# Kernel optimization log

Hardware: AMD Instinct MI355X
Metric: run time of the kernel (lower is better)

The kernel has to match this reference:

```python
import jax, jax.numpy as jnp
import numpy as np

B, T, C, H = 2, 2048, 1024, 16
D = C // H  # head dim 64

def setup_inputs() -> dict:
    key = jax.random.key(0)
    k1, k2, k3 = jax.random.split(key, 3)
    x = jax.random.normal(k1, (B, T, C), dtype=jnp.float32)
    W_attn = jax.random.normal(k2, (C, 3 * C), dtype=jnp.float32) * (1.0 / np.sqrt(C))
    b_attn = jnp.zeros((3 * C,), dtype=jnp.float32)
    W_proj = jax.random.normal(k3, (C, C), dtype=jnp.float32) * (1.0 / np.sqrt(C))
    b_proj = jnp.zeros((C,), dtype=jnp.float32)
    return {"x": x, "W_attn": W_attn, "b_attn": b_attn, "W_proj": W_proj, "b_proj": b_proj}

def reference(x, W_attn, b_attn, W_proj, b_proj):
    Bsz, Tlen, Cdim = x.shape
    qkv = x @ W_attn + b_attn  # [B,T,3C]
    q, k, v = jnp.split(qkv, 3, axis=2)
    # [B,T,C] -> [B,H,T,D]
    q = q.reshape(Bsz, Tlen, H, D).transpose(0, 2, 1, 3)
    k = k.reshape(Bsz, Tlen, H, D).transpose(0, 2, 1, 3)
    v = v.reshape(Bsz, Tlen, H, D).transpose(0, 2, 1, 3)
    att = jnp.einsum('bhqd,bhkd->bhqk', q, k) * (1.0 / np.sqrt(D))
    causal = jnp.tril(jnp.ones((Tlen, Tlen), dtype=bool))
    att = jnp.where(causal[None, None, :, :], att, jnp.float32(-jnp.inf))
    att = jax.nn.softmax(att, axis=-1)
    y = jnp.einsum('bhqk,bhkd->bhqd', att, v)  # [B,H,T,D]
    y = y.transpose(0, 2, 1, 3).reshape(Bsz, Tlen, Cdim)
    return y @ W_proj + b_proj
```

## Files before the change

kernel.cpp:

```cpp
#include <hip/hip_runtime.h>
#include <math.h>

#define BSZ 2
#define TSEQ 2048
#define CDIM 1024
#define HNUM 16

typedef __attribute__((ext_vector_type(8))) short bhalf8;
typedef __attribute__((ext_vector_type(4))) short bhalf4;
typedef __attribute__((ext_vector_type(4))) float floatx4;

__device__ __forceinline__ unsigned short f2bf(float f) {
    union { float f; unsigned u; } v;
    v.f = f;
    unsigned r = v.u + 0x7FFFu + ((v.u >> 16) & 1u);
    return (unsigned short)(r >> 16);
}

__device__ __forceinline__ floatx4 fx4_zero() { floatx4 z = {0.f,0.f,0.f,0.f}; return z; }

typedef __attribute__((address_space(3))) unsigned int lds_u32;
typedef const __attribute__((address_space(1))) unsigned int g_u32;
__device__ __forceinline__ void async_copy16(const void* g, void* l) {
    __builtin_amdgcn_global_load_lds((g_u32*)g, (lds_u32*)l, 16, 0, 0);
}

__device__ __forceinline__ void trans_tile(
    const float* __restrict__ W, unsigned short* __restrict__ Wt,
    int K, int N, int n0, int k0, int tid, float (*t)[33])
{
    const int tx = tid & 31, ty = tid >> 5;
#pragma unroll
    for (int i = 0; i < 4; ++i)
        t[ty + i * 8][tx] = W[(size_t)(k0 + ty + i * 8) * N + n0 + tx];
    __syncthreads();
#pragma unroll
    for (int i = 0; i < 4; ++i)
        Wt[(size_t)(n0 + ty + i * 8) * K + k0 + tx] = f2bf(t[tx][ty + i * 8]);
}

__global__ __launch_bounds__(256) void prepass(
    const float* __restrict__ x, unsigned short* __restrict__ xb,
    const float* __restrict__ Wa, unsigned short* __restrict__ WtA,
    const float* __restrict__ Wp, unsigned short* __restrict__ WtP)
{
    __shared__ float t[32][33];
    const int bid = blockIdx.x;
    const int tid = threadIdx.x;
    if (bid < 2048) {
        size_t i = ((size_t)bid * 256 + tid) * 8;
        float4 a = *(const float4*)(x + i);
        float4 b = *(const float4*)(x + i + 4);
        uint4 o;
        o.x = (unsigned)f2bf(a.x) | ((unsigned)f2bf(a.y) << 16);
        o.y = (unsigned)f2bf(a.z) | ((unsigned)f2bf(a.w) << 16);
        o.z = (unsigned)f2bf(b.x) | ((unsigned)f2bf(b.y) << 16);
        o.w = (unsigned)f2bf(b.z) | ((unsigned)f2bf(b.w) << 16);
        *(uint4*)(xb + i) = o;
    } else if (bid < 5120) {
        int tl = bid - 2048;
        trans_tile(Wa, WtA, 1024, 3072, (tl % 96) * 32, (tl / 96) * 32, tid, t);
    } else {
        int tl = bid - 5120;
        trans_tile(Wp, WtP, 1024, 1024, (tl % 32) * 32, (tl / 32) * 32, tid, t);
    }
}

template<int BM, int BN, int BK, bool OUT_BF16>
__global__ __launch_bounds__(256) void gemm_bt(
    const unsigned short* __restrict__ A, const unsigned short* __restrict__ Bt,
    const float* __restrict__ bias, void* __restrict__ Cp,
    int M, int N, int K, int v_start, unsigned short* __restrict__ vt, int q_end)
{
    constexpr int ALINES = (BM * BK) / 2048;
    constexpr int BLINES = (BN * BK) / 2048;
    constexpr int MT = BM / 32;
    constexpr int NT = BN / 32;
    constexpr int KK = BK / 32;
    constexpr int CPR = BK / 8;
    __shared__ unsigned short As[2][BM * BK];
    __shared__ unsigned short Bs[2][BN * BK];

    const int tid   = threadIdx.x;
    const int nx  = (int)gridDim.x;
    const int lin = (int)(blockIdx.y * gridDim.x + blockIdx.x);
    const int cpx = (int)(gridDim.x * gridDim.y) >> 3;
    const int swz = (lin & 7) * cpx + (lin >> 3);
    const int bn  = swz % nx;
    const int bm  = swz / nx;

    const int wave  = tid >> 6;
    const int col16 = tid & 15;
    const int quad  = (tid & 63) >> 4;
    const int wm    = (wave >> 1) * (BM / 2);
    const int wn    = (wave & 1) * (BN / 2);

    floatx4 acc[MT][NT];
#pragma unroll
    for (int i = 0; i < MT; ++i)
#pragma unroll
        for (int j = 0; j < NT; ++j) acc[i][j] = fx4_zero();

    const int gr = tid / CPR;
    const int cq = tid % CPR;
    const int gk = (BK == 32)
        ? (((cq + 4 - ((gr >> 1) & 3)) & 3) * 8)
        : ((cq ^ (gr & 7)) * 8);
    const unsigned short* Ab = A  + (size_t)(bm * BM + gr) * K + gk;
    const unsigned short* Bb = Bt + (size_t)(bn * BN + gr) * K + gk;
    constexpr int RPL = 2048 / BK;

#define STAGE(k0, bf) { \
    char* AsB = (char*)As[bf] + wave * 1024; \
    char* BsB = (char*)Bs[bf] + wave * 1024; \
    _Pragma("unroll") \
    for (int l = 0; l < ALINES; ++l) \
        async_copy16(Ab + (size_t)l * RPL * K + (k0), AsB + l * 4096); \
    _Pragma("unroll") \
    for (int l = 0; l < BLINES; ++l) \
        async_copy16(Bb + (size_t)l * RPL * K + (k0), BsB + l * 4096); }

#define COMPUTE(bf) { \
    _Pragma("unroll") \
    for (int kk = 0; kk < KK; ++kk) { \
        const int sw8 = (BK == 32) \
            ? (((quad + (col16 >> 1)) & 3) * 8) \
            : ((((kk << 2) + quad) ^ (col16 & 7)) * 8); \
        bhalf8 a[MT], b[NT]; \
        _Pragma("unroll") \
        for (int i = 0; i < MT; ++i) \
            a[i] = *(const bhalf8*)&As[bf][(wm + i * 16 + col16) * BK + sw8]; \
        _Pragma("unroll") \
        for (int j = 0; j < NT; ++j) \
            b[j] = *(const bhalf8*)&Bs[bf][(wn + j * 16 + col16) * BK + sw8]; \
        _Pragma("unroll") \
        for (int i = 0; i < MT; ++i) \
            _Pragma("unroll") \
            for (int j = 0; j < NT; ++j) \
                acc[i][j] = __builtin_amdgcn_mfma_f32_16x16x32_bf16(a[i], b[j], acc[i][j], 0, 0, 0); \
    } }

    STAGE(0, 0);
    __syncthreads();
    int buf = 0;
    for (int k0 = 0; k0 < K - BK; k0 += BK) {
        STAGE(k0 + BK, buf ^ 1);
        COMPUTE(buf);
        __syncthreads();
        buf ^= 1;
    }
    COMPUTE(buf);
#undef STAGE
#undef COMPUTE

    const int colbase = bn * BN + wn;
    const bool vpath = (v_start >= 0) && (colbase >= v_start);
    const float csc = (colbase < q_end) ? 0.18033688f : 1.0f;
#pragma unroll
    for (int j = 0; j < NT; ++j) {
        int col = colbase + j * 16 + col16;
        float bv = bias[col];
#pragma unroll
        for (int i = 0; i < MT; ++i) {
            if (vpath) {
                int row0 = bm * BM + wm + i * 16 + quad * 4;
                ushort4 o;
                o.x = f2bf((acc[i][j][0] + bv) * csc);
                o.y = f2bf((acc[i][j][1] + bv) * csc);
                o.z = f2bf((acc[i][j][2] + bv) * csc);
                o.w = f2bf((acc[i][j][3] + bv) * csc);
                size_t vrow = (size_t)((row0 >> 11) * 1024 + (col - v_start));
                *(ushort4*)(vt + vrow * 2048 + (row0 & 2047)) = o;
            } else {
#pragma unroll
                for (int r = 0; r < 4; ++r) {
                    int row = bm * BM + wm + i * 16 + quad * 4 + r;
                    float v = (acc[i][j][r] + bv) * csc;
                    if (OUT_BF16)
                        ((unsigned short*)Cp)[(size_t)row * N + col] = f2bf(v);
                    else
                        ((float*)Cp)[(size_t)row * N + col] = v;
                }
            }
        }
    }
}

template<bool DIAG>
__device__ __forceinline__ void attn_tile(
    const unsigned short* __restrict__ Ks, const unsigned short* __restrict__ Vt,
    const bhalf8* qf, floatx4* oT, floatx4& accl,
    int col16, int quad, int qloc)
{
    const int sx = col16 & 7;
    const floatx4 minusC = {-17.31234049f, -17.31234049f, -17.31234049f, -17.31234049f};
    const bhalf4 ones = {0x3F80, 0x3F80, 0x3F80, 0x3F80};

    floatx4 s[4];
#pragma unroll
    for (int n = 0; n < 4; ++n) {
        const int row = 16 * n + col16;
        bhalf8 k0 = *(const bhalf8*)&Ks[row * 64 + ((quad ^ sx) * 8)];
        bhalf8 k1 = *(const bhalf8*)&Ks[row * 64 + (((4 + quad) ^ sx) * 8)];
        floatx4 t = __builtin_amdgcn_mfma_f32_16x16x32_bf16(k0, qf[0], minusC, 0, 0, 0);
        s[n] = __builtin_amdgcn_mfma_f32_16x16x32_bf16(k1, qf[1], t, 0, 0, 0);
    }

    bhalf4 pb[4];
#pragma unroll
    for (int n = 0; n < 4; ++n) {
        unsigned a[4];
#pragma unroll
        for (int r = 0; r < 4; ++r) {
            float p = exp2f(s[n][r]);
            if (DIAG) {
                if (16 * n + quad * 4 + r > qloc) p = 0.f;
            }
            a[r] = __float_as_uint(p) + 0x8000u;
        }
        union { unsigned u[2]; bhalf4 b; } uu;
        uu.u[0] = (a[0] >> 16) | (a[1] & 0xffff0000u);
        uu.u[1] = (a[2] >> 16) | (a[3] & 0xffff0000u);
        pb[n] = uu.b;
        accl = __builtin_amdgcn_mfma_f32_16x16x16bf16_1k(ones, pb[n], accl, 0, 0, 0);
    }

#pragma unroll
    for (int n = 0; n < 4; ++n) {
#pragma unroll
        for (int dt = 0; dt < 4; ++dt) {
            const int d = 16 * dt + col16;
            const bhalf4 av = *(const bhalf4*)&Vt[d * 76 + 16 * n + quad * 4];
            oT[dt] = __builtin_amdgcn_mfma_f32_16x16x16bf16_1k(av, pb[n], oT[dt], 0, 0, 0);
        }
    }
}

__global__ __launch_bounds__(256) void attn_mfma(
    const unsigned short* __restrict__ qkv,
    const unsigned short* __restrict__ vT,
    unsigned short* __restrict__ yout)
{
    __shared__ unsigned short Kbuf[2][64 * 64];
    __shared__ unsigned short Vbuf[2][64 * 76];

    const int tid   = threadIdx.x;
    const int wave  = tid >> 6;
    const int col16 = tid & 15;
    const int quad  = (tid & 63) >> 4;

    const int y = (int)blockIdx.y;
    const int g = y >> 3, r = y & 7;
    const int qb = (g == 0) ? 31 - r : (g == 1) ? r : (g == 2) ? 23 - r : 8 + r;

    const int bh    = blockIdx.x;
    const int b     = bh >> 4;
    const int h     = bh & 15;

    const unsigned short* base  = qkv + (size_t)b * TSEQ * 3072 + h * 64;
    const unsigned short* kbase = base + CDIM;
    const unsigned short* vtb   = vT + (size_t)(b * 1024 + h * 64) * 2048;

    bhalf8 qf[2];
    {
        const unsigned short* qrow =
            base + (size_t)(qb * 64 + wave * 16 + col16) * 3072 + quad * 8;
        qf[0] = *(const bhalf8*)qrow;
        qf[1] = *(const bhalf8*)(qrow + 32);
    }

    const int krow = tid >> 3;
    const int kchk = (tid & 7) ^ (krow & 7);
    const unsigned short* ksrc0 = kbase + (size_t)krow * 3072 + kchk * 8;
    const unsigned short* ksrc1 = kbase + (size_t)(krow + 32) * 3072 + kchk * 8;

    const int vd  = tid >> 3;
    const int vt0 = (tid & 7) * 8;
    const unsigned short* vsrc0 = vtb + (size_t)vd * 2048 + vt0;
    const unsigned short* vsrc1 = vtb + (size_t)(vd + 32) * 2048 + vt0;

#define KSTAGE(kb, bf) { \
    char* Kd = (char*)Kbuf[bf] + wave * 1024; \
    async_copy16(ksrc0 + (size_t)(kb) * 64 * 3072, Kd); \
    async_copy16(ksrc1 + (size_t)(kb) * 64 * 3072, Kd + 4096); }

    floatx4 oT[4];
#pragma unroll
    for (int dt = 0; dt < 4; ++dt) oT[dt] = fx4_zero();
    floatx4 accl = fx4_zero();
    const int qloc = wave * 16 + col16;

    {
        uint4 nv0 = *(const uint4*)vsrc0;
        uint4 nv1 = *(const uint4*)vsrc1;
        KSTAGE(0, 0);
        *(uint4*)&Vbuf[0][vd * 76 + vt0]        = nv0;
        *(uint4*)&Vbuf[0][(vd + 32) * 76 + vt0] = nv1;
    }
    __syncthreads();
    int buf = 0;
    for (int kb = 0; kb < qb; ++kb) {
        uint4 nv0 = *(const uint4*)(vsrc0 + (size_t)(kb + 1) * 64);
        uint4 nv1 = *(const uint4*)(vsrc1 + (size_t)(kb + 1) * 64);
        KSTAGE(kb + 1, buf ^ 1);
        attn_tile<false>(Kbuf[buf], Vbuf[buf], qf, oT, accl, col16, quad, qloc);
        *(uint4*)&Vbuf[buf ^ 1][vd * 76 + vt0]        = nv0;
        *(uint4*)&Vbuf[buf ^ 1][(vd + 32) * 76 + vt0] = nv1;
        __syncthreads();
        buf ^= 1;
    }
    attn_tile<true>(Kbuf[buf], Vbuf[buf], qf, oT, accl, col16, quad, qloc);
#undef KSTAGE

    const float inv = 1.0f / accl[0];
    const size_t row = (size_t)b * TSEQ + (size_t)qb * 64 + wave * 16 + col16;
#pragma unroll
    for (int dt = 0; dt < 4; ++dt) {
        ushort4 o;
        o.x = f2bf(oT[dt][0] * inv);
        o.y = f2bf(oT[dt][1] * inv);
        o.z = f2bf(oT[dt][2] * inv);
        o.w = f2bf(oT[dt][3] * inv);
        *(ushort4*)(yout + row * CDIM + h * 64 + 16 * dt + quad * 4) = o;
    }
}

extern "C" void kernel_launch(void* const* d_in, const int* in_sizes, int n_in,
                              void* d_out, int out_size, void* d_ws, size_t ws_size,
                              hipStream_t stream)
{
    const float* x      = (const float*)d_in[0];
    const float* W_attn = (const float*)d_in[1];
    const float* b_attn = (const float*)d_in[2];
    const float* W_proj = (const float*)d_in[3];
    const float* b_proj = (const float*)d_in[4];
    float* out = (float*)d_out;

    unsigned short* qkv = (unsigned short*)d_ws;
    unsigned short* y   = qkv + (size_t)4096 * 3072;
    unsigned short* xb  = y   + (size_t)4096 * 1024;
    unsigned short* WtA = xb  + (size_t)4096 * 1024;
    unsigned short* WtP = WtA + (size_t)3072 * 1024;
    unsigned short* vT  = WtP + (size_t)1024 * 1024;

    prepass<<<dim3(6144), 256, 0, stream>>>(x, xb, W_attn, WtA, W_proj, WtP);

    gemm_bt<128, 128, 32, true><<<dim3(3072 / 128, 4096 / 128), 256, 0, stream>>>(
        xb, WtA, b_attn, qkv, 4096, 3072, 1024, 2048, vT, 1024);

    attn_mfma<<<dim3(BSZ * HNUM, TSEQ / 64), 256, 0, stream>>>(qkv, vT, y);

    gemm_bt<64, 128, 64, false><<<dim3(1024 / 128, 4096 / 64), 256, 0, stream>>>(
        y, WtP, b_proj, out, 4096, 1024, 1024, -1, nullptr, 0);
}
```

Baseline: 175.1 us.

## Process two query tiles per attention block to reuse staged K/V tiles

After: 193.3 us. 10.4% more time.

```diff
diff --git a/kernel.cpp b/kernel.cpp
--- a/kernel.cpp
+++ b/kernel.cpp
@@ -186,43 +186,60 @@
     }
 }
 
-template<bool DIAG>
-__device__ __forceinline__ void attn_tile(
+template<int MODE>
+__device__ __forceinline__ void attn_tile2(
     const unsigned short* __restrict__ Ks, const unsigned short* __restrict__ Vt,
-    const bhalf8* qf, floatx4* oT, floatx4& accl,
+    const bhalf8* qfA, const bhalf8* qfB,
+    floatx4* oTA, floatx4* oTB, floatx4& acclA, floatx4& acclB,
     int col16, int quad, int qloc)
 {
     const int sx = col16 & 7;
     const floatx4 minusC = {-17.31234049f, -17.31234049f, -17.31234049f, -17.31234049f};
     const bhalf4 ones = {0x3F80, 0x3F80, 0x3F80, 0x3F80};
 
-    floatx4 s[4];
+    floatx4 sA[4], sB[4];
 #pragma unroll
     for (int n = 0; n < 4; ++n) {
         const int row = 16 * n + col16;
         bhalf8 k0 = *(const bhalf8*)&Ks[row * 64 + ((quad ^ sx) * 8)];
         bhalf8 k1 = *(const bhalf8*)&Ks[row * 64 + (((4 + quad) ^ sx) * 8)];
-        floatx4 t = __builtin_amdgcn_mfma_f32_16x16x32_bf16(k0, qf[0], minusC, 0, 0, 0);
-        s[n] = __builtin_amdgcn_mfma_f32_16x16x32_bf16(k1, qf[1], t, 0, 0, 0);
-    }
-
-    bhalf4 pb[4];
+        if (MODE != 2) {
+            floatx4 t = __builtin_amdgcn_mfma_f32_16x16x32_bf16(k0, qfA[0], minusC, 0, 0, 0);
+            sA[n] = __builtin_amdgcn_mfma_f32_16x16x32_bf16(k1, qfA[1], t, 0, 0, 0);
+        }
+        floatx4 u = __builtin_amdgcn_mfma_f32_16x16x32_bf16(k0, qfB[0], minusC, 0, 0, 0);
+        sB[n] = __builtin_amdgcn_mfma_f32_16x16x32_bf16(k1, qfB[1], u, 0, 0, 0);
+    }
+
+    bhalf4 pbA[4], pbB[4];
 #pragma unroll
     for (int n = 0; n < 4; ++n) {
-        unsigned a[4];
+        if (MODE != 2) {
+            unsigned a[4];
+#pragma unroll
+            for (int r = 0; r < 4; ++r) {
+                float p = exp2f(sA[n][r]);
+                if (MODE == 1) { if (16 * n + quad * 4 + r > qloc) p = 0.f; }
+                a[r] = __float_as_uint(p) + 0x8000u;
+            }
+            union { unsigned u[2]; bhalf4 b; } ua;
+            ua.u[0] = (a[0] >> 16) | (a[1] & 0xffff0000u);
+            ua.u[1] = (a[2] >> 16) | (a[3] & 0xffff0000u);
+            pbA[n] = ua.b;
+            acclA = __builtin_amdgcn_mfma_f32_16x16x16bf16_1k(ones, pbA[n], acclA, 0, 0, 0);
+        }
+        unsigned c[4];
 #pragma unroll
         for (int r = 0; r < 4; ++r) {
-            float p = exp2f(s[n][r]);
-            if (DIAG) {
-                if (16 * n + quad * 4 + r > qloc) p = 0.f;
-            }
-            a[r] = __float_as_uint(p) + 0x8000u;
-        }
-        union { unsigned u[2]; bhalf4 b; } uu;
-        uu.u[0] = (a[0] >> 16) | (a[1] & 0xffff0000u);
-        uu.u[1] = (a[2] >> 16) | (a[3] & 0xffff0000u);
-        pb[n] = uu.b;
-        accl = __builtin_amdgcn_mfma_f32_16x16x16bf16_1k(ones, pb[n], accl, 0, 0, 0);
+            float p = exp2f(sB[n][r]);
+            if (MODE == 2) { if (16 * n + quad * 4 + r > qloc) p = 0.f; }
+            c[r] = __float_as_uint(p) + 0x8000u;
+        }
+        union { unsigned u[2]; bhalf4 b; } ub;
+        ub.u[0] = (c[0] >> 16) | (c[1] & 0xffff0000u);
+        ub.u[1] = (c[2] >> 16) | (c[3] & 0xffff0000u);
+        pbB[n] = ub.b;
+        acclB = __builtin_amdgcn_mfma_f32_16x16x16bf16_1k(ones, pbB[n], acclB, 0, 0, 0);
     }
 
 #pragma unroll
@@ -231,7 +248,9 @@
         for (int dt = 0; dt < 4; ++dt) {
             const int d = 16 * dt + col16;
             const bhalf4 av = *(const bhalf4*)&Vt[d * 76 + 16 * n + quad * 4];
-            oT[dt] = __builtin_amdgcn_mfma_f32_16x16x16bf16_1k(av, pb[n], oT[dt], 0, 0, 0);
+            if (MODE != 2)
+                oTA[dt] = __builtin_amdgcn_mfma_f32_16x16x16bf16_1k(av, pbA[n], oTA[dt], 0, 0, 0);
+            oTB[dt] = __builtin_amdgcn_mfma_f32_16x16x16bf16_1k(av, pbB[n], oTB[dt], 0, 0, 0);
         }
     }
 }
@@ -250,23 +269,25 @@
     const int quad  = (tid & 63) >> 4;
 
     const int y = (int)blockIdx.y;
-    const int g = y >> 3, r = y & 7;
-    const int qb = (g == 0) ? 31 - r : (g == 1) ? r : (g == 2) ? 23 - r : 8 + r;
-
-    const int bh    = blockIdx.x;
-    const int b     = bh >> 4;
-    const int h     = bh & 15;
+    const int Q = (y < 8) ? 15 - y : y - 8;
+
+    const int bh = blockIdx.x;
+    const int b  = bh >> 4;
+    const int h  = bh & 15;
 
     const unsigned short* base  = qkv + (size_t)b * TSEQ * 3072 + h * 64;
     const unsigned short* kbase = base + CDIM;
     const unsigned short* vtb   = vT + (size_t)(b * 1024 + h * 64) * 2048;
 
-    bhalf8 qf[2];
+    bhalf8 qfA[2], qfB[2];
     {
-        const unsigned short* qrow =
-            base + (size_t)(qb * 64 + wave * 16 + col16) * 3072 + quad * 8;
-        qf[0] = *(const bhalf8*)qrow;
-        qf[1] = *(const bhalf8*)(qrow + 32);
+        const unsigned short* qrowA =
+            base + (size_t)(Q * 128 + wave * 16 + col16) * 3072 + quad * 8;
+        qfA[0] = *(const bhalf8*)qrowA;
+        qfA[1] = *(const bhalf8*)(qrowA + 32);
+        const unsigned short* qrowB = qrowA + (size_t)64 * 3072;
+        qfB[0] = *(const bhalf8*)qrowB;
+        qfB[1] = *(const bhalf8*)(qrowB + 32);
     }
 
     const int krow = tid >> 3;
@@ -284,10 +305,10 @@
     async_copy16(ksrc0 + (size_t)(kb) * 64 * 3072, Kd); \
     async_copy16(ksrc1 + (size_t)(kb) * 64 * 3072, Kd + 4096); }
 
-    floatx4 oT[4];
-#pragma unroll
-    for (int dt = 0; dt < 4; ++dt) oT[dt] = fx4_zero();
-    floatx4 accl = fx4_zero();
+    floatx4 oTA[4], oTB[4];
+#pragma unroll
+    for (int dt = 0; dt < 4; ++dt) { oTA[dt] = fx4_zero(); oTB[dt] = fx4_zero(); }
+    floatx4 acclA = fx4_zero(), acclB = fx4_zero();
     const int qloc = wave * 16 + col16;
 
     {
@@ -299,29 +320,50 @@
     }
     __syncthreads();
     int buf = 0;
-    for (int kb = 0; kb < qb; ++kb) {
+    const int kd = 2 * Q;
+    for (int kb = 0; kb < kd; ++kb) {
         uint4 nv0 = *(const uint4*)(vsrc0 + (size_t)(kb + 1) * 64);
         uint4 nv1 = *(const uint4*)(vsrc1 + (size_t)(kb + 1) * 64);
         KSTAGE(kb + 1, buf ^ 1);
-        attn_tile<false>(Kbuf[buf], Vbuf[buf], qf, oT, accl, col16, quad, qloc);
+        attn_tile2<0>(Kbuf[buf], Vbuf[buf], qfA, qfB, oTA, oTB, acclA, acclB,
+                      col16, quad, qloc);
         *(uint4*)&Vbuf[buf ^ 1][vd * 76 + vt0]        = nv0;
         *(uint4*)&Vbuf[buf ^ 1][(vd + 32) * 76 + vt0] = nv1;
         __syncthreads();
         buf ^= 1;
     }
-    attn_tile<true>(Kbuf[buf], Vbuf[buf], qf, oT, accl, col16, quad, qloc);
+    {
+        uint4 nv0 = *(const uint4*)(vsrc0 + (size_t)(kd + 1) * 64);
+        uint4 nv1 = *(const uint4*)(vsrc1 + (size_t)(kd + 1) * 64);
+        KSTAGE(kd + 1, buf ^ 1);
+        attn_tile2<1>(Kbuf[buf], Vbuf[buf], qfA, qfB, oTA, oTB, acclA, acclB,
+                      col16, quad, qloc);
+        *(uint4*)&Vbuf[buf ^ 1][vd * 76 + vt0]        = nv0;
+        *(uint4*)&Vbuf[buf ^ 1][(vd + 32) * 76 + vt0] = nv1;
+        __syncthreads();
+        buf ^= 1;
+    }
+    attn_tile2<2>(Kbuf[buf], Vbuf[buf], qfA, qfB, oTA, oTB, acclA, acclB,
+                  col16, quad, qloc);
 #undef KSTAGE
 
-    const float inv = 1.0f / accl[0];
-    const size_t row = (size_t)b * TSEQ + (size_t)qb * 64 + wave * 16 + col16;
+    const float invA = 1.0f / acclA[0];
+    const float invB = 1.0f / acclB[0];
+    const size_t rowA = (size_t)b * TSEQ + (size_t)Q * 128 + wave * 16 + col16;
+    const size_t rowB = rowA + 64;
 #pragma unroll
     for (int dt = 0; dt < 4; ++dt) {
-        ushort4 o;
-        o.x = f2bf(oT[dt][0] * inv);
-        o.y = f2bf(oT[dt][1] * inv);
-        o.z = f2bf(oT[dt][2] * inv);
-        o.w = f2bf(oT[dt][3] * inv);
-        *(ushort4*)(yout + row * CDIM + h * 64 + 16 * dt + quad * 4) = o;
+        ushort4 oA, oB;
+        oA.x = f2bf(oTA[dt][0] * invA);
+        oA.y = f2bf(oTA[dt][1] * invA);
+        oA.z = f2bf(oTA[dt][2] * invA);
+        oA.w = f2bf(oTA[dt][3] * invA);
+        oB.x = f2bf(oTB[dt][0] * invB);
+        oB.y = f2bf(oTB[dt][1] * invB);
+        oB.z = f2bf(oTB[dt][2] * invB);
+        oB.w = f2bf(oTB[dt][3] * invB);
+        *(ushort4*)(yout + rowA * CDIM + h * 64 + 16 * dt + quad * 4) = oA;
+        *(ushort4*)(yout + rowB * CDIM + h * 64 + 16 * dt + quad * 4) = oB;
     }
 }
 
@@ -348,7 +390,7 @@
     gemm_bt<128, 128, 32, true><<<dim3(3072 / 128, 4096 / 128), 256, 0, stream>>>(
         xb, WtA, b_attn, qkv, 4096, 3072, 1024, 2048, vT, 1024);
 
-    attn_mfma<<<dim3(BSZ * HNUM, TSEQ / 64), 256, 0, stream>>>(qkv, vT, y);
+    attn_mfma<<<dim3(BSZ * HNUM, TSEQ / 128), 256, 0, stream>>>(qkv, vT, y);
 
     gemm_bt<64, 128, 64, false><<<dim3(1024 / 128, 4096 / 64), 256, 0, stream>>>(
         y, WtP, b_proj, out, 4096, 1024, 1024, -1, nullptr, 0);
```
